# Kernel optimization log

Hardware: AMD Instinct MI355X
Metric: run time of the kernel (lower is better)

The kernel has to match this reference:

```python
import jax, jax.numpy as jnp
import numpy as np
from jax import lax

B, S, D, G, V = 32, 8, 128, 32, 64   # batch, slots, hidden_dim, grid_size, vocab_size
K, ED = 128, 32                       # VQ codebook size, code dim


def _conv(x, w, b, pad):
    # standard Conv2d, NCHW / OIHW
    y = lax.conv_general_dilated(x, w, (1, 1), [(pad, pad), (pad, pad)],
                                 dimension_numbers=('NCHW', 'OIHW', 'NCHW'))
    return y + b[None, :, None, None]


def _convT(x, w, b):
    # ConvTranspose2d(k=5, stride=1, padding=2) == conv with spatially flipped
    # kernel, padding k-1-p = 2, channels swapped (IOHW layout of torch weight).
    y = lax.conv_general_dilated(x, jnp.flip(w, (2, 3)), (1, 1), [(2, 2), (2, 2)],
                                 dimension_numbers=('NCHW', 'IOHW', 'NCHW'))
    return y + b[None, :, None, None]


def _build_grid(h, w):
    ys = jnp.linspace(0.0, 1.0, h)
    xs = jnp.linspace(0.0, 1.0, w)
    gy, gx = jnp.meshgrid(ys, xs, indexing='ij')
    g = jnp.stack([gy, gx], axis=-1)                 # [H,W,2]
    return jnp.concatenate([g, 1.0 - g], axis=-1)    # [H,W,4]


def setup_inputs() -> dict:
    key = jax.random.key(0)
    ks = jax.random.split(key, 20)
    sc = 0.05
    n = lambda k, sh: jax.random.normal(k, sh, jnp.float32) * sc
    return {
        'latent': jax.random.normal(ks[0], (B, S, D), jnp.float32),
        'pos_w': n(ks[1], (D, 4)),            # Linear(4, hidden): [out,in]
        'pos_b': jnp.zeros((D,), jnp.float32),
        'ct1_w': n(ks[2], (D, 64, 5, 5)),     # ConvTranspose2d: [in,out,kH,kW]
        'ct1_b': jnp.zeros((64,), jnp.float32),
        'ct2_w': n(ks[3], (64, 32, 5, 5)),
        'ct2_b': jnp.zeros((32,), jnp.float32),
        'codebook': jax.random.uniform(ks[4], (K, ED), jnp.float32, -1.0 / K, 1.0 / K),
        'c1_w': n(ks[5], (64, 32, 3, 3)),     # Conv2d: [out,in,kH,kW]
        'c1_b': jnp.zeros((64,), jnp.float32),
        'c2_w': n(ks[6], (V, 64, 3, 3)),
        'c2_b': jnp.zeros((V,), jnp.float32),
        'a1_w': n(ks[7], (64, 32, 3, 3)),
        'a1_b': jnp.zeros((64,), jnp.float32),
        'a2_w': n(ks[8], (1, 64, 3, 3)),
        'a2_b': jnp.zeros((1,), jnp.float32),
    }


def _forward(latent, pos_w, pos_b, ct1_w, ct1_b, ct2_w, ct2_b, codebook,
             c1_w, c1_b, c2_w, c2_b, a1_w, a1_b, a2_w, a2_b):
    b, s, d = latent.shape
    # spatial broadcast of slot latents -> [B*S, D, H, W]
    z = jnp.broadcast_to(latent.reshape(b * s, d, 1, 1), (b * s, d, G, G))
    # soft position embedding
    grid = _build_grid(G, G)                                  # [H,W,4]
    pos = (grid @ pos_w.T + pos_b).transpose(2, 0, 1)[None]   # [1,D,H,W]
    z = z + pos
    # ConvTranspose decoder
    h = jax.nn.relu(_convT(z, ct1_w, ct1_b))
    feat = jax.nn.relu(_convT(h, ct2_w, ct2_b))               # [B*S,32,H,W]
    # VQ bottleneck on channel-last features
    fp = feat.transpose(0, 2, 3, 1)                           # [B*S,H,W,32]
    flat = fp.reshape(-1, ED)                                 # [N,32]
    dist = (jnp.sum(flat * flat, axis=1, keepdims=True)
            + jnp.sum(codebook * codebook, axis=1)
            - 2.0 * flat @ codebook.T)                        # [N,K]
    idx = jnp.argmin(dist, axis=1)                            # [N]
    q = codebook[idx].reshape(fp.shape)                       # gather lookup
    e_loss = jnp.mean((lax.stop_gradient(q) - fp) ** 2)
    q_loss = jnp.mean((q - lax.stop_gradient(fp)) ** 2)
    vq_loss = q_loss + 0.25 * e_loss
    q_ste = fp + lax.stop_gradient(q - fp)                    # straight-through
    vq_feat = q_ste.transpose(0, 3, 1, 2)                     # [B*S,32,H,W]
    # heads
    colors = _conv(jax.nn.silu(_conv(vq_feat, c1_w, c1_b, 1)), c2_w, c2_b, 1)
    colors = colors.reshape(b, s, V, G, G)
    alphas = _conv(jax.nn.silu(_conv(feat, a1_w, a1_b, 1)), a2_w, a2_b, 1)
    alphas = alphas.reshape(b, s, 1, G, G)
    alphas_n = jax.nn.softmax(alphas, axis=1)
    recon = jnp.sum(alphas_n * colors, axis=1)                # [B,V,H,W]
    return recon, alphas_n, vq_loss


def reference(latent, pos_w, pos_b, ct1_w, ct1_b, ct2_w, ct2_b, codebook,
              c1_w, c1_b, c2_w, c2_b, a1_w, a1_b, a2_w, a2_b):
    return _forward(latent, pos_w, pos_b, ct1_w, ct1_b, ct2_w, ct2_b, codebook,
                    c1_w, c1_b, c2_w, c2_b, a1_w, a1_b, a2_w, a2_b)
```

## Files before the change

kernel.cpp:

```cpp
#include <hip/hip_runtime.h>
#include <math.h>

#define AOFF 2097152
#define LOFF 2359296

typedef __attribute__((ext_vector_type(8))) short short8;
typedef __attribute__((ext_vector_type(4))) float f32x4;

__device__ __forceinline__ int clsf(int v) { return v < 2 ? v : (v > 29 ? v - 27 : 2); }

__device__ __forceinline__ unsigned int f2bfu(float x) {
    unsigned int u = __float_as_uint(x);
    return (u + 0x7FFFu + ((u >> 16) & 1u)) >> 16;
}
__device__ __forceinline__ unsigned int cvt2(float a, float b) {
    return f2bfu(a) | (f2bfu(b) << 16);
}
__device__ __forceinline__ float bf2f(unsigned short u) {
    return __uint_as_float(((unsigned int)u) << 16);
}

__global__ void w1t_kernel(const float* __restrict__ w1, float* __restrict__ w1t) {
    int idx = blockIdx.x * 256 + threadIdx.x;
    if (idx >= 204800) return;
    int tap = idx % 25, rest = idx / 25;
    w1t[tap * 8192 + rest] = w1[idx];
}

__global__ void tapabc_kernel(const float* __restrict__ pw, const float* __restrict__ pb,
                              const float* __restrict__ w1t, float* __restrict__ tapabc) {
    __shared__ float A3[384];
    int tap = blockIdx.x, t = threadIdx.x;
    if (t < 128) {
        float p0 = pw[t * 4], p1 = pw[t * 4 + 1], p2 = pw[t * 4 + 2], p3 = pw[t * 4 + 3];
        A3[t] = p2 + p3 + pb[t];
        A3[128 + t] = p0 - p2;
        A3[256 + t] = p1 - p3;
    }
    __syncthreads();
    int o = t & 63, comp = t >> 6;
    const float* wp = w1t + tap * 8192 + o;
    const float* a = A3 + comp * 128;
    float s = 0.f;
    for (int i = 0; i < 128; ++i) s = fmaf(wp[i * 64], a[i], s);
    tapabc[(tap * 64 + o) * 3 + comp] = s;
}

__global__ void pfill_kernel(const float* __restrict__ tapabc, const float* __restrict__ b1,
                             float* __restrict__ P2) {
    __shared__ float uv[75];
    int o = blockIdx.x, t = threadIdx.x;
    if (t < 75) {
        int cls = t / 3, comp = t % 3;
        int cy = cls / 5, cx = cls % 5;
        const int klo[5] = {2, 1, 0, 0, 0}, khi[5] = {4, 4, 4, 3, 2};
        const float inv31 = 1.f / 31.f;
        float s = (comp == 0) ? b1[o] : 0.f;
        for (int ky = klo[cy]; ky <= khi[cy]; ++ky)
            for (int kx = klo[cx]; kx <= khi[cx]; ++kx) {
                int tap = (4 - ky) * 5 + (4 - kx);
                const float* tp = &tapabc[(tap * 64 + o) * 3];
                if (comp == 0) s += tp[0] + tp[1] * (ky - 2) * inv31 + tp[2] * (kx - 2) * inv31;
                else if (comp == 1) s += tp[1] * inv31;
                else s += tp[2] * inv31;
            }
        uv[t] = s;
    }
    __syncthreads();
    int y = t >> 5, x = t & 31;
    int cls = clsf(y) * 5 + clsf(x);
    float val = uv[cls * 3] + uv[cls * 3 + 1] * y + uv[cls * 3 + 2] * x;
    P2[((o >> 1) << 11) + (t << 1) + (o & 1)] = val;
}

__global__ void wsum_kernel(const float* __restrict__ w1, float* __restrict__ Wsum) {
    int idx = blockIdx.x * 256 + threadIdx.x;
    if (idx >= 25 * 128 * 64) return;
    int cls = idx >> 13;
    int i = (idx >> 6) & 127;
    int o = idx & 63;
    int cy = cls / 5, cx = cls % 5;
    const int klo[5] = {2, 1, 0, 0, 0}, khi[5] = {4, 4, 4, 3, 2};
    float s = 0.f;
    for (int ky = klo[cy]; ky <= khi[cy]; ++ky)
        for (int kx = klo[cx]; kx <= khi[cx]; ++kx)
            s += w1[(i * 64 + o) * 25 + (4 - ky) * 5 + (4 - kx)];
    Wsum[idx] = s;
}

__global__ void m_kernel(const float* __restrict__ latent, const float* __restrict__ Wsum,
                         float* __restrict__ M) {
    int n = blockIdx.x, cls = blockIdx.y, o = threadIdx.x;
    const float* l = &latent[n * 128];
    const float* w = &Wsum[cls * 8192 + o];
    float a0 = 0.f, a1 = 0.f;
    for (int i = 0; i < 128; i += 2) {
        a0 = fmaf(l[i], w[i * 64], a0);
        a1 = fmaf(l[i + 1], w[(i + 1) * 64], a1);
    }
    M[(n * 25 + cls) * 64 + o] = a0 + a1;
}

__global__ void prep_all_kernel(const float* __restrict__ a1w, const float* __restrict__ c1w,
                                const float* __restrict__ c2w, const float* __restrict__ ct2w,
                                short* __restrict__ wtall) {
    int gid = blockIdx.x * 256 + threadIdx.x;
    if (gid < 36864) {
        const float* src = gid < 18432 ? a1w : c1w;
        int idx = gid < 18432 ? gid : gid - 18432;
        int j = idx & 7, fi = idx >> 3;
        int o = fi % 64, g = (fi / 64) & 3, t = fi / 256;
        int i = g * 8 + j;
        wtall[gid] = (short)f2bfu(src[(o * 32 + i) * 9 + (t / 3) * 3 + (t % 3)]);
    } else if (gid < 73728) {
        int idx = gid - 36864;
        int j = idx & 7, fi = idx >> 3;
        int o = fi % 64, g = (fi / 64) & 3, ks = (fi / 256) & 1, t = fi / 512;
        int i = ks * 32 + g * 8 + j;
        wtall[gid] = (short)f2bfu(c2w[(o * 64 + i) * 9 + (t / 3) * 3 + (t % 3)]);
    } else if (gid < 124928) {
        int idx = gid - 73728;
        int j = idx & 7, fi = idx >> 3;
        int o = fi & 31, g = (fi >> 5) & 3, ks = (fi >> 7) & 1, t = fi >> 8;
        int i = ks * 32 + g * 8 + j;
        int ky = t / 5, kx = t % 5;
        wtall[gid] = (short)f2bfu(ct2w[((i * 32 + o) * 5 + (4 - ky)) * 5 + (4 - kx)]);
    }
}

__global__ __launch_bounds__(256) void conv5_kernel(
        const float* __restrict__ M, const float* __restrict__ P2,
        const short* __restrict__ wt, const float* __restrict__ b2,
        unsigned short* __restrict__ featb) {
    __shared__ __align__(16) short tile[12 * 36 * 40];
    __shared__ float Ml[1600];
    const int n = blockIdx.x, y0 = blockIdx.y * 8;
    const int tid = threadIdx.x, w = tid >> 6, l = tid & 63;
    const int lx = l & 15, lg = l >> 4;

    for (int e = tid; e < 1600; e += 256) Ml[e] = M[n * 1600 + e];
    __syncthreads();

    f32x4 acc[2][2][2];
    #pragma unroll
    for (int m = 0; m < 2; ++m)
        #pragma unroll
        for (int q = 0; q < 2; ++q)
            #pragma unroll
            for (int c = 0; c < 2; ++c) acc[m][q][c] = (f32x4){0.f, 0.f, 0.f, 0.f};

    #pragma unroll 1
    for (int ks = 0; ks < 2; ++ks) {
        if (ks) __syncthreads();
        for (int e = tid; e < 6912; e += 256) {
            int cx = e % 36;
            int q = e / 36;
            int ipl = q & 15;
            int r = q >> 4;
            int gy = y0 - 2 + r, gx = cx - 2;
            unsigned int pack = 0u;
            if (gy >= 0 && gy < 32 && gx >= 0 && gx < 32) {
                int cls = clsf(gy) * 5 + clsf(gx);
                int pp = gy * 32 + gx;
                float2 pv = ((const float2*)P2)[((ks * 16 + ipl) << 10) + pp];
                float2 ml = ((const float2*)Ml)[cls * 32 + ks * 16 + ipl];
                pack = cvt2(fmaxf(ml.x + pv.x, 0.f), fmaxf(ml.y + pv.y, 0.f));
            }
            *(unsigned int*)((char*)tile + (r * 36 + cx) * 80 + ipl * 4) = pack;
        }
        __syncthreads();
        for (int kx = 0; kx < 5; ++kx) {
            short8 af[5][2];
            #pragma unroll
            for (int ky = 0; ky < 5; ++ky)
                #pragma unroll
                for (int m = 0; m < 2; ++m)
                    af[ky][m] = *(const short8*)(wt + (ky * 5 + kx) * 2048 +
                                                 ((ks * 4 + lg) * 32 + m * 16 + lx) * 8);
            #pragma unroll
            for (int colf = 0; colf < 2; ++colf) {
                const int cbase = ((2 * w) * 36 + kx + colf * 16 + lx) * 80 + lg * 16;
                short8 bc[6];
                #pragma unroll
                for (int ir = 0; ir < 6; ++ir)
                    bc[ir] = *(const short8*)((char*)tile + cbase + ir * (36 * 80));
                #pragma unroll
                for (int ky = 0; ky < 5; ++ky)
                    #pragma unroll
                    for (int q = 0; q < 2; ++q)
                        #pragma unroll
                        for (int m = 0; m < 2; ++m)
                            acc[m][q][colf] = __builtin_amdgcn_mfma_f32_16x16x32_bf16(
                                af[ky][m], bc[q + ky], acc[m][q][colf], 0, 0, 0);
            }
        }
    }

    #pragma unroll
    for (int m = 0; m < 2; ++m)
        #pragma unroll
        for (int q = 0; q < 2; ++q)
            #pragma unroll
            for (int colf = 0; colf < 2; ++colf) {
                int yl = 2 * w + q, x = colf * 16 + lx;
                unsigned long long pk = 0ull;
                #pragma unroll
                for (int r = 0; r < 4; ++r) {
                    int och = m * 16 + lg * 4 + r;
                    float v = fmaxf(acc[m][q][colf][r] + b2[och], 0.f);
                    pk |= (unsigned long long)f2bfu(v) << (16 * r);
                }
                *(unsigned long long*)(featb + (n * 1024 + (y0 + yl) * 32 + x) * 32
                                       + m * 16 + lg * 4) = pk;
            }
}

template<int I, int O, int ACT>
__global__ __launch_bounds__(256) void conv3_kernel(
        const unsigned short* __restrict__ in_, const short* __restrict__ wt,
        const float* __restrict__ bias, unsigned short* __restrict__ out_) {
    constexpr int KS = I / 32, MF = O / 16;
    constexpr int ABUF = KS * 4 * O * 8;
    __shared__ __align__(16) short smem[10 * 34 * 40];
    const int n = blockIdx.x, y0 = blockIdx.y * 8;
    const int tid = threadIdx.x, w = tid >> 6, l = tid & 63;
    const int lx = l & 15, lg = l >> 4;

    f32x4 acc[MF][2][2];
    #pragma unroll
    for (int m = 0; m < MF; ++m)
        #pragma unroll
        for (int q = 0; q < 2; ++q)
            #pragma unroll
            for (int c = 0; c < 2; ++c) acc[m][q][c] = (f32x4){0.f, 0.f, 0.f, 0.f};

    #pragma unroll 1
    for (int ks = 0; ks < KS; ++ks) {
        if (ks) __syncthreads();
        for (int e = tid; e < 1360; e += 256) {
            int px = e >> 2, qc = e & 3;
            int r = px / 34, cx = px - r * 34;
            int gy = y0 - 1 + r, gx = cx - 1;
            short8 v8 = (short8){0, 0, 0, 0, 0, 0, 0, 0};
            if (gy >= 0 && gy < 32 && gx >= 0 && gx < 32)
                v8 = *(const short8*)(in_ + (n * 1024 + gy * 32 + gx) * I + ks * 32 + qc * 8);
            *(short8*)((char*)smem + px * 80 + qc * 16) = v8;
        }
        __syncthreads();
        for (int kx = 0; kx < 3; ++kx) {
            short8 af[3][MF];
            #pragma unroll
            for (int ky = 0; ky < 3; ++ky)
                #pragma unroll
                for (int m = 0; m < MF; ++m)
                    af[ky][m] = *(const short8*)(wt + (ky * 3 + kx) * ABUF +
                                                 ((ks * 4 + lg) * O + m * 16 + lx) * 8);
            #pragma unroll
            for (int colf = 0; colf < 2; ++colf) {
                const int cbase = ((2 * w) * 34 + kx + colf * 16 + lx) * 80 + lg * 16;
                short8 bc[4];
                #pragma unroll
                for (int ir = 0; ir < 4; ++ir)
                    bc[ir] = *(const short8*)((char*)smem + cbase + ir * (34 * 80));
                #pragma unroll
                for (int ky = 0; ky < 3; ++ky)
                    #pragma unroll
                    for (int q = 0; q < 2; ++q)
                        #pragma unroll
                        for (int m = 0; m < MF; ++m)
                            acc[m][q][colf] = __builtin_amdgcn_mfma_f32_16x16x32_bf16(
                                af[ky][m], bc[q + ky], acc[m][q][colf], 0, 0, 0);
            }
        }
    }

    #pragma unroll
    for (int m = 0; m < MF; ++m)
        #pragma unroll
        for (int q = 0; q < 2; ++q)
            #pragma unroll
            for (int colf = 0; colf < 2; ++colf) {
                int yl = 2 * w + q, x = colf * 16 + lx;
                unsigned long long pk = 0ull;
                #pragma unroll
                for (int r = 0; r < 4; ++r) {
                    int och = m * 16 + lg * 4 + r;
                    float v = acc[m][q][colf][r] + bias[och];
                    if (ACT == 1) v = v / (1.f + expf(-v));
                    pk |= (unsigned long long)f2bfu(v) << (16 * r);
                }
                *(unsigned long long*)(out_ + (n * 1024 + (y0 + yl) * 32 + x) * O
                                       + m * 16 + lg * 4) = pk;
            }
}

__global__ void a2dot_kernel(const unsigned short* __restrict__ in, const float* __restrict__ w,
                             float* __restrict__ s9) {
    __shared__ float wl[576];
    int t = threadIdx.x;
    for (int e = t; e < 576; e += 256) wl[e] = w[e];
    __syncthreads();
    int p = blockIdx.x * 256 + t;
    float acc[9];
    #pragma unroll
    for (int k = 0; k < 9; ++k) acc[k] = 0.f;
    const unsigned short* ip = in + (long long)p * 64;
    #pragma unroll
    for (int c8 = 0; c8 < 8; ++c8) {
        short8 v8 = *(const short8*)(ip + c8 * 8);
        #pragma unroll
        for (int j = 0; j < 8; ++j) {
            float v = bf2f((unsigned short)v8[j]);
            #pragma unroll
            for (int k = 0; k < 9; ++k) acc[k] = fmaf(v, wl[(c8 * 8 + j) * 9 + k], acc[k]);
        }
    }
    #pragma unroll
    for (int k = 0; k < 9; ++k) s9[(k << 18) + p] = acc[k];
}

__global__ void a2soft_kernel(const float* __restrict__ s9, const float* __restrict__ b2,
                              float* __restrict__ outp) {
    int idx = blockIdx.x * 256 + threadIdx.x;
    if (idx >= 32 * 1024) return;
    int bb = idx >> 10, yx = idx & 1023;
    int y = yx >> 5, x = yx & 31;
    float v[8];
    float bias = b2[0];
    #pragma unroll
    for (int s = 0; s < 8; ++s) {
        int n = bb * 8 + s;
        float a = bias;
        #pragma unroll
        for (int ky = 0; ky < 3; ++ky) {
            int yy = y + ky - 1;
            if (yy < 0 || yy > 31) continue;
            #pragma unroll
            for (int kx = 0; kx < 3; ++kx) {
                int xx = x + kx - 1;
                if (xx < 0 || xx > 31) continue;
                a += s9[((ky * 3 + kx) << 18) + (n << 10) + yy * 32 + xx];
            }
        }
        v[s] = a;
    }
    float m = -3.4e38f;
    #pragma unroll
    for (int s = 0; s < 8; ++s) m = fmaxf(m, v[s]);
    float sum = 0.f;
    #pragma unroll
    for (int s = 0; s < 8; ++s) { v[s] = expf(v[s] - m); sum += v[s]; }
    float inv = 1.f / sum;
    #pragma unroll
    for (int s = 0; s < 8; ++s) outp[AOFF + ((bb * 8 + s) << 10) + yx] = v[s] * inv;
}

__global__ __launch_bounds__(256) void vq_mfma_kernel(
        const unsigned short* __restrict__ featb, const float* __restrict__ codebook,
        unsigned short* __restrict__ qfeat, float* __restrict__ partial) {
    __shared__ float cbf[4096];
    __shared__ __align__(16) short cbh[4096];
    __shared__ float cn[128];
    __shared__ float red[4];
    const int tid = threadIdx.x;
    const int w = tid >> 6, l = tid & 63;
    const int lx = l & 15, lg = l >> 4;

    for (int e = tid; e < 4096; e += 256) {
        float v = codebook[e];
        cbf[e] = v;
        int code = e >> 5, d = e & 31;
        int off = (code * 32 + d) * 2;
        off ^= (code & 7) << 4;
        *(short*)((char*)cbh + off) = (short)f2bfu(v);
    }
    __syncthreads();
    if (tid < 128) {
        float s = 0.f;
        #pragma unroll
        for (int c = 0; c < 32; ++c) { float v = cbf[tid * 32 + c]; s = fmaf(v, v, s); }
        cn[tid] = s;
    }
    short8 af[8];
    #pragma unroll
    for (int m = 0; m < 8; ++m) {
        int code = m * 16 + lx;
        int off = (code * 32 + lg * 8) * 2;
        off ^= (code & 7) << 4;
        af[m] = *(const short8*)((char*)cbh + off);
    }
    __syncthreads();
    float cnh[8][4];
    #pragma unroll
    for (int m = 0; m < 8; ++m)
        #pragma unroll
        for (int r = 0; r < 4; ++r)
            cnh[m][r] = 0.5f * cn[m * 16 + lg * 4 + r];

    const int n = blockIdx.x >> 2;
    const int yxw = (blockIdx.x & 3) * 256 + w * 64;
    float lloss = 0.f;

    #pragma unroll 1
    for (int pxg = 0; pxg < 4; ++pxg) {
        int yx = yxw + pxg * 16 + lx;
        short8 bbs = *(const short8*)(featb + (n * 1024 + yx) * 32 + lg * 8);
        f32x4 S[8];
        #pragma unroll
        for (int m = 0; m < 8; ++m)
            S[m] = __builtin_amdgcn_mfma_f32_16x16x32_bf16(
                af[m], bbs, (f32x4){0.f, 0.f, 0.f, 0.f}, 0, 0, 0);
        float bestv = -3.4e38f; int besti = 0;
        #pragma unroll
        for (int m = 0; m < 8; ++m)
            #pragma unroll
            for (int r = 0; r < 4; ++r) {
                float v = S[m][r] - cnh[m][r];
                int code = m * 16 + lg * 4 + r;
                if (v > bestv) { bestv = v; besti = code; }
            }
        #pragma unroll
        for (int d = 16; d < 64; d <<= 1) {
            float ov = __shfl_xor(bestv, d);
            int oi = __shfl_xor(besti, d);
            if (ov > bestv || (ov == bestv && oi < besti)) { bestv = ov; besti = oi; }
        }
        int offq = (besti * 32 + lg * 8) * 2;
        offq ^= (besti & 7) << 4;
        short8 qh = *(const short8*)((char*)cbh + offq);
        *(short8*)(qfeat + (n * 1024 + yx) * 32 + lg * 8) = qh;
        const float* qf = &cbf[besti * 32 + lg * 8];
        #pragma unroll
        for (int j = 0; j < 8; ++j) {
            float fv = bf2f((unsigned short)bbs[j]);
            float dd = qf[j] - fv;
            lloss = fmaf(dd, dd, lloss);
        }
    }
    for (int off = 32; off > 0; off >>= 1) lloss += __shfl_down(lloss, off);
    if (l == 0) red[w] = lloss;
    __syncthreads();
    if (tid == 0) partial[blockIdx.x] = (red[0] + red[1]) + (red[2] + red[3]);
}

__global__ __launch_bounds__(256) void recon_kernel(
        const unsigned short* __restrict__ colors, float* __restrict__ outp) {
    const int b = blockIdx.x, y8 = blockIdx.y;
    const int tid = threadIdx.x;
    const int yxl = tid & 127, vh = tid >> 7;
    const int yx = y8 * 128 + yxl;
    float acc[32];
    #pragma unroll
    for (int v = 0; v < 32; ++v) acc[v] = 0.f;
    #pragma unroll 1
    for (int s = 0; s < 8; ++s) {
        float a = outp[AOFF + ((b * 8 + s) << 10) + yx];
        const unsigned short* cp = colors + ((b * 8 + s) * 1024 + yx) * 64 + vh * 32;
        #pragma unroll
        for (int k = 0; k < 4; ++k) {
            short8 v8 = *(const short8*)(cp + k * 8);
            #pragma unroll
            for (int j = 0; j < 8; ++j)
                acc[k * 8 + j] = fmaf(a, bf2f((unsigned short)v8[j]), acc[k * 8 + j]);
        }
    }
    #pragma unroll
    for (int v = 0; v < 32; ++v)
        outp[(b * 64 + vh * 32 + v) * 1024 + yx] = acc[v];
}

__global__ void loss_kernel(const float* __restrict__ partial, float* __restrict__ outp) {
    __shared__ float red[4];
    int t = threadIdx.x;
    float s = 0.f;
    for (int i = t; i < 1024; i += 256) s += partial[i];
    for (int o = 32; o > 0; o >>= 1) s += __shfl_down(s, o);
    if ((t & 63) == 0) red[t >> 6] = s;
    __syncthreads();
    if (t == 0) outp[LOFF] = 1.25f * ((red[0] + red[1]) + (red[2] + red[3])) / 8388608.0f;
}

extern "C" void kernel_launch(void* const* d_in, const int* in_sizes, int n_in,
                              void* d_out, int out_size, void* d_ws, size_t ws_size,
                              hipStream_t stream) {
    const float* latent  = (const float*)d_in[0];
    const float* pos_w   = (const float*)d_in[1];
    const float* pos_b   = (const float*)d_in[2];
    const float* ct1_w   = (const float*)d_in[3];
    const float* ct1_b   = (const float*)d_in[4];
    const float* ct2_w   = (const float*)d_in[5];
    const float* ct2_b   = (const float*)d_in[6];
    const float* codebook= (const float*)d_in[7];
    const float* c1_w    = (const float*)d_in[8];
    const float* c1_b    = (const float*)d_in[9];
    const float* c2_w    = (const float*)d_in[10];
    const float* c2_b    = (const float*)d_in[11];
    const float* a1_w    = (const float*)d_in[12];
    const float* a1_b    = (const float*)d_in[13];
    const float* a2_w    = (const float*)d_in[14];
    const float* a2_b    = (const float*)d_in[15];
    float* out = (float*)d_out;

    float* ws     = (float*)d_ws;
    unsigned short* featb = (unsigned short*)ws;
    float* s9     = ws + 8388608;
    float* tapabc = s9 + 2359296;
    float* P      = tapabc + 4800;
    float* M      = P + 65536;
    float* partial= M + 409600;
    float* w1t    = partial + 1024;
    float* Wsum   = w1t + 204800;
    short* wtall  = (short*)(Wsum + 204800);
    short* wtA    = wtall;
    short* wtC1   = wtall + 18432;
    short* wtC2   = wtall + 36864;
    short* wtT2   = wtall + 73728;
    unsigned short* tmpb    = (unsigned short*)(wtall + 124928);
    unsigned short* qfeatb  = tmpb + 16777216;
    unsigned short* colorsb = qfeatb + 8388608;

    w1t_kernel<<<800, 256, 0, stream>>>(ct1_w, w1t);
    tapabc_kernel<<<25, 192, 0, stream>>>(pos_w, pos_b, w1t, tapabc);
    pfill_kernel<<<64, 1024, 0, stream>>>(tapabc, ct1_b, P);
    wsum_kernel<<<800, 256, 0, stream>>>(ct1_w, Wsum);
    m_kernel<<<dim3(256, 25), 64, 0, stream>>>(latent, Wsum, M);
    prep_all_kernel<<<488, 256, 0, stream>>>(a1_w, c1_w, c2_w, ct2_w, wtall);

    conv5_kernel<<<dim3(256, 4), 256, 0, stream>>>(M, P, wtT2, ct2_b, featb);
    conv3_kernel<32, 64, 1><<<dim3(256, 4), 256, 0, stream>>>(featb, wtA, a1_b, tmpb);
    a2dot_kernel<<<1024, 256, 0, stream>>>(tmpb, a2_w, s9);
    a2soft_kernel<<<128, 256, 0, stream>>>(s9, a2_b, out);
    vq_mfma_kernel<<<1024, 256, 0, stream>>>(featb, codebook, qfeatb, partial);
    conv3_kernel<32, 64, 1><<<dim3(256, 4), 256, 0, stream>>>(qfeatb, wtC1, c1_b, tmpb);
    conv3_kernel<64, 64, 0><<<dim3(256, 4), 256, 0, stream>>>(tmpb, wtC2, c2_b, colorsb);
    recon_kernel<<<dim3(32, 8), 256, 0, stream>>>(colorsb, out);
    loss_kernel<<<1, 256, 0, stream>>>(partial, out);
}
```

Baseline: 222.7 us.

## Software-pipeline 3x3 conv input staging via registers and process two images per block

Replaces the generic templated conv3 kernel with two specialized kernels. The 32-channel conv processes two images per block, double-buffering the second image's halo tile through registers and LDS while the first is computed. The 64-channel conv preloads both 32-channel halves into registers up front, which removes the global-load latency between the two K-slices. This targets the exposed global-load latency before the MFMA loops, at the cost of higher register pressure and double the LDS for the two-image kernel.

```diff
diff --git a/kernel.cpp b/kernel.cpp
--- a/kernel.cpp
+++ b/kernel.cpp
@@ -215,67 +215,234 @@
             }
 }
 
-template<int I, int O, int ACT>
-__global__ __launch_bounds__(256) void conv3_kernel(
+__device__ __forceinline__ void conv3_core(
+        const short* __restrict__ tile, const short* __restrict__ wt, int abase,
+        f32x4 (&acc)[4][2][2], int w, int lx, int lg) {
+    #pragma unroll
+    for (int kx = 0; kx < 3; ++kx) {
+        short8 af[3][4];
+        #pragma unroll
+        for (int ky = 0; ky < 3; ++ky)
+            #pragma unroll
+            for (int m = 0; m < 4; ++m)
+                af[ky][m] = *(const short8*)(wt + (ky * 3 + kx) * abase +
+                                             (lg * 64 + m * 16 + lx) * 8);
+        #pragma unroll
+        for (int colf = 0; colf < 2; ++colf) {
+            const int cbase = ((2 * w) * 34 + kx + colf * 16 + lx) * 80 + lg * 16;
+            short8 bc[4];
+            #pragma unroll
+            for (int ir = 0; ir < 4; ++ir)
+                bc[ir] = *(const short8*)((const char*)tile + cbase + ir * (34 * 80));
+            #pragma unroll
+            for (int ky = 0; ky < 3; ++ky)
+                #pragma unroll
+                for (int q = 0; q < 2; ++q)
+                    #pragma unroll
+                    for (int m = 0; m < 4; ++m)
+                        acc[m][q][colf] = __builtin_amdgcn_mfma_f32_16x16x32_bf16(
+                            af[ky][m], bc[q + ky], acc[m][q][colf], 0, 0, 0);
+        }
+    }
+}
+
+__device__ __forceinline__ void conv3_epi(
+        f32x4 (&acc)[4][2][2], const float* __restrict__ bias,
+        unsigned short* __restrict__ out_, int n, int y0, int w, int lx, int lg, int act) {
+    #pragma unroll
+    for (int m = 0; m < 4; ++m)
+        #pragma unroll
+        for (int q = 0; q < 2; ++q)
+            #pragma unroll
+            for (int colf = 0; colf < 2; ++colf) {
+                int yl = 2 * w + q, x = colf * 16 + lx;
+                unsigned long long pk = 0ull;
+                #pragma unroll
+                for (int r = 0; r < 4; ++r) {
+                    int och = m * 16 + lg * 4 + r;
+                    float v = acc[m][q][colf][r] + bias[och];
+                    if (act) v = v / (1.f + expf(-v));
+                    pk |= (unsigned long long)f2bfu(v) << (16 * r);
+                }
+                *(unsigned long long*)(out_ + (n * 1024 + (y0 + yl) * 32 + x) * 64
+                                       + m * 16 + lg * 4) = pk;
+            }
+}
+
+template<int ACT>
+__global__ __launch_bounds__(256) void conv3d_kernel(
         const unsigned short* __restrict__ in_, const short* __restrict__ wt,
         const float* __restrict__ bias, unsigned short* __restrict__ out_) {
-    constexpr int KS = I / 32, MF = O / 16;
-    constexpr int ABUF = KS * 4 * O * 8;
+    __shared__ __align__(16) short tileA[10 * 34 * 40];
+    __shared__ __align__(16) short tileB[10 * 34 * 40];
+    const int n0 = blockIdx.x * 2, y0 = blockIdx.y * 8;
+    const int tid = threadIdx.x, w = tid >> 6, l = tid & 63;
+    const int lx = l & 15, lg = l >> 4;
+
+    short8 rA[6], rB[6];
+    int pxv[6], qcv[6];
+    #pragma unroll
+    for (int it = 0; it < 6; ++it) {
+        int e = tid + it * 256;
+        short8 v8 = (short8){0, 0, 0, 0, 0, 0, 0, 0};
+        int px = e >> 2, qc = e & 3;
+        pxv[it] = px; qcv[it] = qc;
+        if (e < 1360) {
+            int r = px / 34, cx = px - r * 34;
+            int gy = y0 - 1 + r, gx = cx - 1;
+            if (gy >= 0 && gy < 32 && gx >= 0 && gx < 32)
+                v8 = *(const short8*)(in_ + (n0 * 1024 + gy * 32 + gx) * 32 + qc * 8);
+        }
+        rA[it] = v8;
+    }
+    #pragma unroll
+    for (int it = 0; it < 6; ++it)
+        if (tid + it * 256 < 1360)
+            *(short8*)((char*)tileA + pxv[it] * 80 + qcv[it] * 16) = rA[it];
+    #pragma unroll
+    for (int it = 0; it < 6; ++it) {
+        int e = tid + it * 256;
+        short8 v8 = (short8){0, 0, 0, 0, 0, 0, 0, 0};
+        if (e < 1360) {
+            int px = pxv[it], qc = qcv[it];
+            int r = px / 34, cx = px - r * 34;
+            int gy = y0 - 1 + r, gx = cx - 1;
+            if (gy >= 0 && gy < 32 && gx >= 0 && gx < 32)
+                v8 = *(const short8*)(in_ + ((n0 + 1) * 1024 + gy * 32 + gx) * 32 + qc * 8);
+        }
+        rB[it] = v8;
+    }
+    __syncthreads();
+
+    f32x4 acc[4][2][2];
+    #pragma unroll
+    for (int m = 0; m < 4; ++m)
+        #pragma unroll
+        for (int q = 0; q < 2; ++q)
+            #pragma unroll
+            for (int c = 0; c < 2; ++c) acc[m][q][c] = (f32x4){0.f, 0.f, 0.f, 0.f};
+    conv3_core(tileA, wt, 2048, acc, w, lx, lg);
+
+    #pragma unroll
+    for (int it = 0; it < 6; ++it)
+        if (tid + it * 256 < 1360)
+            *(short8*)((char*)tileB + pxv[it] * 80 + qcv[it] * 16) = rB[it];
+    conv3_epi(acc, bias, out_, n0, y0, w, lx, lg, ACT);
+    __syncthreads();
+
+    #pragma unroll
+    for (int m = 0; m < 4; ++m)
+        #pragma unroll
+        for (int q = 0; q < 2; ++q)
+            #pragma unroll
+            for (int c = 0; c < 2; ++c) acc[m][q][c] = (f32x4){0.f, 0.f, 0.f, 0.f};
+    conv3_core(tileB, wt, 2048, acc, w, lx, lg);
+    conv3_epi(acc, bias, out_, n0 + 1, y0, w, lx, lg, ACT);
+}
+
+__global__ __launch_bounds__(256) void c2_kernel(
+        const unsigned short* __restrict__ in_, const short* __restrict__ wt,
+        const float* __restrict__ bias, unsigned short* __restrict__ out_) {
     __shared__ __align__(16) short smem[10 * 34 * 40];
     const int n = blockIdx.x, y0 = blockIdx.y * 8;
     const int tid = threadIdx.x, w = tid >> 6, l = tid & 63;
     const int lx = l & 15, lg = l >> 4;
 
-    f32x4 acc[MF][2][2];
-    #pragma unroll
-    for (int m = 0; m < MF; ++m)
-        #pragma unroll
-        for (int q = 0; q < 2; ++q)
-            #pragma unroll
-            for (int c = 0; c < 2; ++c) acc[m][q][c] = (f32x4){0.f, 0.f, 0.f, 0.f};
-
-    #pragma unroll 1
-    for (int ks = 0; ks < KS; ++ks) {
-        if (ks) __syncthreads();
-        for (int e = tid; e < 1360; e += 256) {
-            int px = e >> 2, qc = e & 3;
+    short8 r0[6], r1[6];
+    int pxv[6], qcv[6];
+    #pragma unroll
+    for (int it = 0; it < 6; ++it) {
+        int e = tid + it * 256;
+        int px = e >> 2, qc = e & 3;
+        pxv[it] = px; qcv[it] = qc;
+        short8 v0 = (short8){0, 0, 0, 0, 0, 0, 0, 0};
+        short8 v1 = v0;
+        if (e < 1360) {
             int r = px / 34, cx = px - r * 34;
             int gy = y0 - 1 + r, gx = cx - 1;
-            short8 v8 = (short8){0, 0, 0, 0, 0, 0, 0, 0};
-            if (gy >= 0 && gy < 32 && gx >= 0 && gx < 32)
-                v8 = *(const short8*)(in_ + (n * 1024 + gy * 32 + gx) * I + ks * 32 + qc * 8);
-            *(short8*)((char*)smem + px * 80 + qc * 16) = v8;
-        }
-        __syncthreads();
-        for (int kx = 0; kx < 3; ++kx) {
-            short8 af[3][MF];
+            if (gy >= 0 && gy < 32 && gx >= 0 && gx < 32) {
+                const unsigned short* p = in_ + (n * 1024 + gy * 32 + gx) * 64 + qc * 8;
+                v0 = *(const short8*)p;
+                v1 = *(const short8*)(p + 32);
+            }
+        }
+        r0[it] = v0; r1[it] = v1;
+    }
+    #pragma unroll
+    for (int it = 0; it < 6; ++it)
+        if (tid + it * 256 < 1360)
+            *(short8*)((char*)smem + pxv[it] * 80 + qcv[it] * 16) = r0[it];
+    __syncthreads();
+
+    f32x4 acc[4][2][2];
+    #pragma unroll
+    for (int m = 0; m < 4; ++m)
+        #pragma unroll
+        for (int q = 0; q < 2; ++q)
+            #pragma unroll
+            for (int c = 0; c < 2; ++c) acc[m][q][c] = (f32x4){0.f, 0.f, 0.f, 0.f};
+
+    #pragma unroll
+    for (int kx = 0; kx < 3; ++kx) {
+        short8 af[3][4];
+        #pragma unroll
+        for (int ky = 0; ky < 3; ++ky)
+            #pragma unroll
+            for (int m = 0; m < 4; ++m)
+                af[ky][m] = *(const short8*)(wt + (ky * 3 + kx) * 4096 +
+                                             ((0 * 4 + lg) * 64 + m * 16 + lx) * 8);
+        #pragma unroll
+        for (int colf = 0; colf < 2; ++colf) {
+            const int cbase = ((2 * w) * 34 + kx + colf * 16 + lx) * 80 + lg * 16;
+            short8 bc[4];
+            #pragma unroll
+            for (int ir = 0; ir < 4; ++ir)
+                bc[ir] = *(const short8*)((char*)smem + cbase + ir * (34 * 80));
             #pragma unroll
             for (int ky = 0; ky < 3; ++ky)
                 #pragma unroll
-                for (int m = 0; m < MF; ++m)
-                    af[ky][m] = *(const short8*)(wt + (ky * 3 + kx) * ABUF +
-                                                 ((ks * 4 + lg) * O + m * 16 + lx) * 8);
-            #pragma unroll
-            for (int colf = 0; colf < 2; ++colf) {
-                const int cbase = ((2 * w) * 34 + kx + colf * 16 + lx) * 80 + lg * 16;
-                short8 bc[4];
-                #pragma unroll
-                for (int ir = 0; ir < 4; ++ir)
-                    bc[ir] = *(const short8*)((char*)smem + cbase + ir * (34 * 80));
-                #pragma unroll
-                for (int ky = 0; ky < 3; ++ky)
+                for (int q = 0; q < 2; ++q)
                     #pragma unroll
-                    for (int q = 0; q < 2; ++q)
-                        #pragma unroll
-                        for (int m = 0; m < MF; ++m)
-                            acc[m][q][colf] = __builtin_amdgcn_mfma_f32_16x16x32_bf16(
-                                af[ky][m], bc[q + ky], acc[m][q][colf], 0, 0, 0);
-            }
-        }
-    }
-
-    #pragma unroll
-    for (int m = 0; m < MF; ++m)
+                    for (int m = 0; m < 4; ++m)
+                        acc[m][q][colf] = __builtin_amdgcn_mfma_f32_16x16x32_bf16(
+                            af[ky][m], bc[q + ky], acc[m][q][colf], 0, 0, 0);
+        }
+    }
+    __syncthreads();
+    #pragma unroll
+    for (int it = 0; it < 6; ++it)
+        if (tid + it * 256 < 1360)
+            *(short8*)((char*)smem + pxv[it] * 80 + qcv[it] * 16) = r1[it];
+    __syncthreads();
+    #pragma unroll
+    for (int kx = 0; kx < 3; ++kx) {
+        short8 af[3][4];
+        #pragma unroll
+        for (int ky = 0; ky < 3; ++ky)
+            #pragma unroll
+            for (int m = 0; m < 4; ++m)
+                af[ky][m] = *(const short8*)(wt + (ky * 3 + kx) * 4096 +
+                                             ((1 * 4 + lg) * 64 + m * 16 + lx) * 8);
+        #pragma unroll
+        for (int colf = 0; colf < 2; ++colf) {
+            const int cbase = ((2 * w) * 34 + kx + colf * 16 + lx) * 80 + lg * 16;
+            short8 bc[4];
+            #pragma unroll
+            for (int ir = 0; ir < 4; ++ir)
+                bc[ir] = *(const short8*)((char*)smem + cbase + ir * (34 * 80));
+            #pragma unroll
+            for (int ky = 0; ky < 3; ++ky)
+                #pragma unroll
+                for (int q = 0; q < 2; ++q)
+                    #pragma unroll
+                    for (int m = 0; m < 4; ++m)
+                        acc[m][q][colf] = __builtin_amdgcn_mfma_f32_16x16x32_bf16(
+                            af[ky][m], bc[q + ky], acc[m][q][colf], 0, 0, 0);
+        }
+    }
+
+    #pragma unroll
+    for (int m = 0; m < 4; ++m)
         #pragma unroll
         for (int q = 0; q < 2; ++q)
             #pragma unroll
@@ -286,10 +453,9 @@
                 for (int r = 0; r < 4; ++r) {
                     int och = m * 16 + lg * 4 + r;
                     float v = acc[m][q][colf][r] + bias[och];
-                    if (ACT == 1) v = v / (1.f + expf(-v));
                     pk |= (unsigned long long)f2bfu(v) << (16 * r);
                 }
-                *(unsigned long long*)(out_ + (n * 1024 + (y0 + yl) * 32 + x) * O
+                *(unsigned long long*)(out_ + (n * 1024 + (y0 + yl) * 32 + x) * 64
                                        + m * 16 + lg * 4) = pk;
             }
 }
@@ -527,12 +693,12 @@
     prep_all_kernel<<<488, 256, 0, stream>>>(a1_w, c1_w, c2_w, ct2_w, wtall);
 
     conv5_kernel<<<dim3(256, 4), 256, 0, stream>>>(M, P, wtT2, ct2_b, featb);
-    conv3_kernel<32, 64, 1><<<dim3(256, 4), 256, 0, stream>>>(featb, wtA, a1_b, tmpb);
+    conv3d_kernel<1><<<dim3(128, 4), 256, 0, stream>>>(featb, wtA, a1_b, tmpb);
     a2dot_kernel<<<1024, 256, 0, stream>>>(tmpb, a2_w, s9);
     a2soft_kernel<<<128, 256, 0, stream>>>(s9, a2_b, out);
     vq_mfma_kernel<<<1024, 256, 0, stream>>>(featb, codebook, qfeatb, partial);
-    conv3_kernel<32, 64, 1><<<dim3(256, 4), 256, 0, stream>>>(qfeatb, wtC1, c1_b, tmpb);
-    conv3_kernel<64, 64, 0><<<dim3(256, 4), 256, 0, stream>>>(tmpb, wtC2, c2_b, colorsb);
+    conv3d_kernel<1><<<dim3(128, 4), 256, 0, stream>>>(qfeatb, wtC1, c1_b, tmpb);
+    c2_kernel<<<dim3(256, 4), 256, 0, stream>>>(tmpb, wtC2, c2_b, colorsb);
     recon_kernel<<<dim3(32, 8), 256, 0, stream>>>(colorsb, out);
     loss_kernel<<<1, 256, 0, stream>>>(partial, out);
 }
```

After: 218.0 us. 2.1% less time.
